# Kernel optimization log

Hardware: AMD Instinct MI355X
Metric: run time of the kernel (lower is better)

## Reference

```python
import jax, jax.numpy as jnp
import numpy as np

B, L, N, P = 64, 512, 321, 720   # batch, seq_len, enc_in, pred_len
E, R, CID, H = 8, 32, 32, 64     # experts, rank, channel_identity_dim, router hidden


def setup_inputs() -> dict:
    key = jax.random.key(0)
    ks = jax.random.split(key, 9)
    return {
        "x": jax.random.normal(ks[0], (B, L, N), dtype=jnp.float32),
        # per-channel identity embedding for the router
        "ident": jax.random.normal(ks[1], (N, CID), dtype=jnp.float32) * 0.02,
        # router MLP: CID -> H -> E
        "rw1": jax.random.normal(ks[2], (CID, H), dtype=jnp.float32) * (1.0 / np.sqrt(CID)),
        "rb1": jnp.zeros((H,), dtype=jnp.float32),
        "rw2": jax.random.normal(ks[3], (H, E), dtype=jnp.float32) * (1.0 / np.sqrt(H)),
        "rb2": jnp.zeros((E,), dtype=jnp.float32),
        # low-rank experts: L -> R -> P
        "w1": jax.random.normal(ks[4], (E, L, R), dtype=jnp.float32) * (1.0 / np.sqrt(L)),
        "w2": jax.random.normal(ks[5], (E, R, P), dtype=jnp.float32) * (1.0 / np.sqrt(R)),
        "b": jnp.zeros((E, P), dtype=jnp.float32),
    }


def reference(x, ident, rw1, rb1, rw2, rb2, w1, w2, b):
    # RevIN-style normalization over the time dim (torch std is unbiased, ddof=1)
    mean = jnp.mean(x, axis=1, keepdims=True)                    # [B,1,N]
    std = jnp.std(x, axis=1, keepdims=True, ddof=1) + 1e-6       # [B,1,N]
    xn = ((x - mean) / std).transpose(0, 2, 1)                   # [B,N,L]

    # per-channel MoE router (soft routing over experts)
    hidden = jax.nn.relu(ident @ rw1 + rb1)                      # [N,H]
    gate = jax.nn.softmax(hidden @ rw2 + rb2, axis=-1)           # [N,E]

    # low-rank expert projections L -> R -> P
    h = jnp.einsum('bnl,elr->bner', xn, w1)                      # [B,N,E,R]
    y = jnp.einsum('bner,erp->bnep', h, w2) + b                  # [B,N,E,P]
    y = jnp.einsum('bnep,ne->bnp', y, gate)                      # [B,N,P]

    pred = y.transpose(0, 2, 1)                                  # [B,P,N]
    return pred * std + mean
```

## Files before the change

kernel.cpp:

```cpp
#include <hip/hip_runtime.h>
#include <math.h>

#define B_ 64
#define L_ 512
#define N_ 321
#define P_ 720
#define E_ 8
#define R_ 32
#define CID_ 32
#define H_ 64
#define ER_ 256
#define KB2 288

typedef __attribute__((ext_vector_type(8))) short bf16x8;
typedef __attribute__((ext_vector_type(4))) float f32x4;
typedef __attribute__((ext_vector_type(8))) unsigned short u16x8;
typedef __attribute__((ext_vector_type(4))) unsigned short u16x4;

#define OFF_GATE 0
#define OFF_CS1  (N_*E_)
#define OFF_W1K  (OFF_CS1 + ER_)
#define OFF_W2X  (OFF_W1K + ER_*L_/2)

__device__ __forceinline__ unsigned short f2bf(float f) {
    unsigned u = __float_as_uint(f);
    u += 0x7fffu + ((u >> 16) & 1u);
    return (unsigned short)(u >> 16);
}
__device__ __forceinline__ float bf2f(unsigned short h) {
    return __uint_as_float(((unsigned)h) << 16);
}

__global__ void router_kernel(const float* __restrict__ ident,
                              const float* __restrict__ rw1, const float* __restrict__ rb1,
                              const float* __restrict__ rw2, const float* __restrict__ rb2,
                              float* __restrict__ gate) {
    int n = blockIdx.x;
    int t = threadIdx.x;
    __shared__ float hid[H_];
    __shared__ float lg[E_];
    float acc = rb1[t];
    #pragma unroll
    for (int c = 0; c < CID_; ++c)
        acc = fmaf(ident[n*CID_ + c], rw1[c*H_ + t], acc);
    hid[t] = fmaxf(acc, 0.f);
    __syncthreads();
    if (t < E_) {
        float a = rb2[t];
        #pragma unroll
        for (int h = 0; h < H_; ++h) a = fmaf(hid[h], rw2[h*E_ + t], a);
        lg[t] = a;
    }
    __syncthreads();
    if (t == 0) {
        float m = lg[0];
        #pragma unroll
        for (int e = 1; e < E_; ++e) m = fmaxf(m, lg[e]);
        float s = 0.f, ex[E_];
        #pragma unroll
        for (int e = 0; e < E_; ++e) { ex[e] = expf(lg[e] - m); s += ex[e]; }
        float inv = 1.f / s;
        #pragma unroll
        for (int e = 0; e < E_; ++e) gate[n*E_ + e] = ex[e] * inv;
    }
}

__global__ void prep_kernel(const float* __restrict__ w1, const float* __restrict__ w2,
                            const float* __restrict__ bias,
                            unsigned short* __restrict__ w1k, unsigned short* __restrict__ w2x,
                            float* __restrict__ cs1) {
    __shared__ float red[16][32];
    int bid = blockIdx.x, t = threadIdx.x;
    if (bid < 256) {
        int g = bid*512 + t;
        int er = g >> 9, l = g & 511;
        w1k[g] = f2bf(w1[(size_t)(er >> 5)*(L_*R_) + (size_t)l*R_ + (er & 31)]);
    } else if (bid < 256 + 720) {
        int p = bid - 256;
        if (t < KB2) {
            unsigned short v;
            if (t < ER_)            v = f2bf(w2[(size_t)t*P_ + p]);
            else if (t < ER_ + E_)  v = f2bf(bias[(size_t)(t - ER_)*P_ + p]);
            else if (t == ER_ + E_) v = 0x3f80;
            else                    v = 0;
            w2x[(size_t)p*KB2 + t] = v;
        }
    } else {
        int e = bid - 976;
        int q = t >> 5, r = t & 31;
        float s = 0.f;
        for (int l = q; l < L_; l += 16)
            s += bf2f(f2bf(w1[(size_t)e*(L_*R_) + (size_t)l*R_ + r]));
        red[q][r] = s;
        __syncthreads();
        if (q == 0) {
            #pragma unroll
            for (int qq = 1; qq < 16; ++qq) s += red[qq][r];
            cs1[e*32 + r] = s;
        }
    }
}

#define HG_STRIDE 296
#define SM_AS   0
#define SM_BS   40960
#define SM_RED  51200
#define SM_MSD  55296
#define SM_OUT  40960
#define SM_TOT  75776

__global__ __launch_bounds__(512, 4) void fused_kernel(
        const float* __restrict__ x, const unsigned short* __restrict__ w1k,
        const unsigned short* __restrict__ w2x, const float* __restrict__ gate,
        const float* __restrict__ cs1, float* __restrict__ out) {
    __shared__ __align__(16) char smem[SM_TOT];
    unsigned short* As  = (unsigned short*)(smem + SM_AS);
    unsigned short* Bs  = (unsigned short*)(smem + SM_BS);
    float* red1 = (float*)(smem + SM_RED);
    float* red2 = red1 + 512;
    float* meanS = (float*)(smem + SM_MSD);
    float* sdS   = meanS + 64;
    unsigned short* hgt = (unsigned short*)(smem + SM_AS);

    const int n0 = blockIdx.x * 64;
    const int b  = blockIdx.y;
    const int tid = threadIdx.x;
    const int lane = tid & 63;
    const int wave = tid >> 6;
    const int wm = wave >> 1;
    const int wn = wave & 1;
    const int l15 = lane & 15;
    const int kgrp = lane >> 4;

    const int arow = tid >> 1;
    const int acol = (tid & 1) * 16;
    const int xn  = tid & 63;
    const int xkb = wave * 4;
    const float* xb = x + (size_t)b * L_ * N_;
    const int gn = n0 + xn;
    const bool nvalid = (gn < N_);

    float s1 = 0.f, s2 = 0.f;
    float xr[3][4];
    u16x8 ar[2][2];

    f32x4 acc[4][2];
    #pragma unroll
    for (int i = 0; i < 4; ++i)
        #pragma unroll
        for (int j = 0; j < 2; ++j) acc[i][j] = (f32x4){0.f,0.f,0.f,0.f};

#define LOADX(s_, t_) { const int k0 = (t_)*32;                                  \
    _Pragma("unroll")                                                            \
    for (int i_ = 0; i_ < 4; ++i_)                                               \
        xr[s_][i_] = nvalid ? xb[(size_t)(k0 + xkb + i_)*N_ + gn] : 0.f; }
#define LOADA(s_, t_) { const int k0 = (t_)*32;                                  \
    ar[s_][0] = *(const u16x8*)&w1k[(size_t)arow*L_ + k0 + acol];                \
    ar[s_][1] = *(const u16x8*)&w1k[(size_t)arow*L_ + k0 + acol + 8]; }
#define STAGE(nb_, xs_, as_) {                                                   \
    *(u16x8*)&As[(size_t)((nb_)*256 + arow)*40 + acol]     = ar[as_][0];         \
    *(u16x8*)&As[(size_t)((nb_)*256 + arow)*40 + acol + 8] = ar[as_][1];         \
    u16x4 bp_;                                                                   \
    _Pragma("unroll")                                                            \
    for (int i_ = 0; i_ < 4; ++i_) {                                             \
        float v_ = xr[xs_][i_]; s1 += v_; s2 = fmaf(v_, v_, s2);                 \
        bp_[i_] = f2bf(v_); }                                                    \
    *(u16x4*)&Bs[(size_t)((nb_)*64 + xn)*40 + xkb] = bp_; }

    LOADX(0, 0); LOADA(0, 0);
    LOADX(1, 1); LOADA(1, 1);
    LOADX(2, 2);
    STAGE(0, 0, 0);
    __syncthreads();

    #pragma unroll
    for (int t = 0; t < 16; ++t) {
        if (t + 3 < 16) LOADX((t + 3) % 3, t + 3);
        if (t + 2 < 16) LOADA((t + 2) & 1, t + 2);
        const int cur = t & 1;
        bf16x8 af[4], bfv[2];
        #pragma unroll
        for (int fm = 0; fm < 4; ++fm)
            af[fm] = *(const bf16x8*)&As[(size_t)(cur*256 + wm*64 + fm*16 + l15)*40 + kgrp*8];
        #pragma unroll
        for (int fn = 0; fn < 2; ++fn)
            bfv[fn] = *(const bf16x8*)&Bs[(size_t)(cur*64 + wn*32 + fn*16 + l15)*40 + kgrp*8];
        #pragma unroll
        for (int fm = 0; fm < 4; ++fm)
            #pragma unroll
            for (int fn = 0; fn < 2; ++fn)
                acc[fm][fn] = __builtin_amdgcn_mfma_f32_16x16x32_bf16(af[fm], bfv[fn], acc[fm][fn], 0, 0, 0);
        if (t < 15) STAGE((t + 1) & 1, (t + 1) % 3, (t + 1) & 1);
        __syncthreads();
    }

    red1[wave*64 + xn] = s1;
    red2[wave*64 + xn] = s2;
    __syncthreads();
    if (tid < 64) {
        float a = 0.f, q = 0.f;
        #pragma unroll
        for (int kk = 0; kk < 8; ++kk) { a += red1[kk*64 + tid]; q += red2[kk*64 + tid]; }
        float mean = a * (1.f/L_);
        float var = (q - (float)L_*mean*mean) * (1.f/(L_-1));
        var = fmaxf(var, 0.f);
        meanS[tid] = mean;
        sdS[tid]   = sqrtf(var) + 1e-6f;
    }
    __syncthreads();

    #pragma unroll
    for (int fm = 0; fm < 4; ++fm) {
        int er0 = wm*64 + fm*16 + kgrp*4;
        int e = er0 >> 5;
        f32x4 c4 = *(const f32x4*)&cs1[er0];
        #pragma unroll
        for (int fn = 0; fn < 2; ++fn) {
            int nl = wn*32 + fn*16 + l15;
            int gnn = n0 + nl; if (gnn > N_-1) gnn = N_-1;
            float g = gate[gnn*E_ + e];
            float m = meanS[nl];
            u16x4 pk;
            #pragma unroll
            for (int j = 0; j < 4; ++j)
                pk[j] = f2bf(g * (acc[fm][fn][j] - m * c4[j]));
            *(u16x4*)&hgt[(size_t)nl*HG_STRIDE + er0] = pk;
        }
    }
    {
        int nl = tid >> 3, seg = tid & 7;
        int gnn = n0 + nl; if (gnn > N_-1) gnn = N_-1;
        float sd = sdS[nl], m = meanS[nl];
        u16x4 pk;
        #pragma unroll
        for (int jj = 0; jj < 4; ++jj) {
            int k = seg*4 + jj;
            float v = (k < E_) ? gate[gnn*E_ + k] * sd : ((k == E_) ? m : 0.f);
            pk[jj] = f2bf(v);
        }
        *(u16x4*)&hgt[(size_t)nl*HG_STRIDE + ER_ + seg*4] = pk;
    }
    __syncthreads();

    float* patch = (float*)(smem + SM_OUT) + wave * 1088;
    for (int pt = wave; pt < 23; pt += 8) {
        const int p0w = pt * 32;
        int pr0 = p0w + l15;       if (pr0 > P_-1) pr0 = P_-1;
        int pr1 = p0w + 16 + l15;  if (pr1 > P_-1) pr1 = P_-1;
        const unsigned short* ap0 = w2x + (size_t)pr0*KB2;
        const unsigned short* ap1 = w2x + (size_t)pr1*KB2;

        f32x4 o[2][4];
        #pragma unroll
        for (int i = 0; i < 2; ++i)
            #pragma unroll
            for (int j = 0; j < 4; ++j) o[i][j] = (f32x4){0.f,0.f,0.f,0.f};

        #pragma unroll
        for (int ks = 0; ks < 9; ++ks) {
            bf16x8 a0f = *(const bf16x8*)&ap0[ks*32 + kgrp*8];
            bf16x8 a1f = *(const bf16x8*)&ap1[ks*32 + kgrp*8];
            bf16x8 bfr[4];
            #pragma unroll
            for (int fn = 0; fn < 4; ++fn)
                bfr[fn] = *(const bf16x8*)&hgt[(size_t)(fn*16 + l15)*HG_STRIDE + ks*32 + kgrp*8];
            #pragma unroll
            for (int fn = 0; fn < 4; ++fn) {
                o[0][fn] = __builtin_amdgcn_mfma_f32_16x16x32_bf16(a0f, bfr[fn], o[0][fn], 0, 0, 0);
                o[1][fn] = __builtin_amdgcn_mfma_f32_16x16x32_bf16(a1f, bfr[fn], o[1][fn], 0, 0, 0);
            }
        }

        #pragma unroll
        for (int fp = 0; fp < 2; ++fp) {
            #pragma unroll
            for (int fn = 0; fn < 4; ++fn)
                #pragma unroll
                for (int j = 0; j < 4; ++j)
                    patch[(kgrp*4 + j)*68 + fn*16 + l15] = o[fp][fn][j];
            __builtin_amdgcn_s_waitcnt(0);
            #pragma unroll
            for (int s = 0; s < 4; ++s) {
                int prow = p0w + fp*16 + 4*s + kgrp;
                f32x4 v = *(const f32x4*)&patch[(4*s + kgrp)*68 + l15*4];
                int nn = n0 + l15*4;
                if (prow < P_) {
                    float* orow = out + ((size_t)b*P_ + prow)*N_;
                    if (nn + 3 < N_) {
                        *(f32x4*)&orow[nn] = v;
                    } else {
                        #pragma unroll
                        for (int q = 0; q < 4; ++q)
                            if (nn + q < N_) orow[nn + q] = v[q];
                    }
                }
            }
        }
    }
#undef LOADX
#undef LOADA
#undef STAGE
}

extern "C" void kernel_launch(void* const* d_in, const int* in_sizes, int n_in,
                              void* d_out, int out_size, void* d_ws, size_t ws_size,
                              hipStream_t stream) {
    const float* x     = (const float*)d_in[0];
    const float* ident = (const float*)d_in[1];
    const float* rw1   = (const float*)d_in[2];
    const float* rb1   = (const float*)d_in[3];
    const float* rw2   = (const float*)d_in[4];
    const float* rb2   = (const float*)d_in[5];
    const float* w1    = (const float*)d_in[6];
    const float* w2    = (const float*)d_in[7];
    const float* bias  = (const float*)d_in[8];
    float* out = (float*)d_out;
    float* ws  = (float*)d_ws;

    float* gate = ws + OFF_GATE;
    float* cs1  = ws + OFF_CS1;
    unsigned short* w1k = (unsigned short*)(ws + OFF_W1K);
    unsigned short* w2x = (unsigned short*)(ws + OFF_W2X);

    router_kernel<<<N_, 64, 0, stream>>>(ident, rw1, rb1, rw2, rb2, gate);
    prep_kernel<<<256 + 720 + 8, 512, 0, stream>>>(w1, w2, bias, w1k, w2x, cs1);
    fused_kernel<<<dim3((N_+63)/64, B_), 512, 0, stream>>>(x, w1k, w2x, gate, cs1, out);
}
```

Before: 69.83 us.

## Swap MFMA operands to store output directly, shrink LDS, remap blocks per XCD

Swaps the A/B operands of the second-stage MFMA so each lane's accumulator holds four consecutive channels. The results can then be written to global memory as float4 without an LDS transpose patch. This removes the patch buffer and overlaps the reduction scratch with the B staging area, cutting LDS from about 74KB to 50KB, and raises launch bounds to 6 blocks per CU. It also flattens the grid and maps blocks so that each XCD handles a contiguous set of batches, which should improve L2 locality. The register pressure of the higher occupancy target may cause spills.

```diff
diff --git a/kernel.cpp b/kernel.cpp
--- a/kernel.cpp
+++ b/kernel.cpp
@@ -104,26 +104,27 @@
 #define HG_STRIDE 296
 #define SM_AS   0
 #define SM_BS   40960
-#define SM_RED  51200
-#define SM_MSD  55296
-#define SM_OUT  40960
-#define SM_TOT  75776
-
-__global__ __launch_bounds__(512, 4) void fused_kernel(
+#define SM_TOT  51200
+
+__global__ __launch_bounds__(512, 6) void fused_kernel(
         const float* __restrict__ x, const unsigned short* __restrict__ w1k,
         const unsigned short* __restrict__ w2x, const float* __restrict__ gate,
         const float* __restrict__ cs1, float* __restrict__ out) {
     __shared__ __align__(16) char smem[SM_TOT];
     unsigned short* As  = (unsigned short*)(smem + SM_AS);
     unsigned short* Bs  = (unsigned short*)(smem + SM_BS);
-    float* red1 = (float*)(smem + SM_RED);
-    float* red2 = red1 + 512;
-    float* meanS = (float*)(smem + SM_MSD);
+    float* red1  = (float*)(smem + SM_BS);
+    float* red2  = red1 + 512;
+    float* meanS = (float*)(smem + SM_BS + 4096);
     float* sdS   = meanS + 64;
     unsigned short* hgt = (unsigned short*)(smem + SM_AS);
 
-    const int n0 = blockIdx.x * 64;
-    const int b  = blockIdx.y;
+    const int bid = blockIdx.x;
+    const int xcd = bid & 7;
+    const int idx = bid >> 3;
+    const int b   = (xcd << 3) + idx / 6;
+    const int n0  = (idx % 6) * 64;
+
     const int tid = threadIdx.x;
     const int lane = tid & 63;
     const int wave = tid >> 6;
@@ -242,13 +243,12 @@
     }
     __syncthreads();
 
-    float* patch = (float*)(smem + SM_OUT) + wave * 1088;
     for (int pt = wave; pt < 23; pt += 8) {
         const int p0w = pt * 32;
         int pr0 = p0w + l15;       if (pr0 > P_-1) pr0 = P_-1;
         int pr1 = p0w + 16 + l15;  if (pr1 > P_-1) pr1 = P_-1;
-        const unsigned short* ap0 = w2x + (size_t)pr0*KB2;
-        const unsigned short* ap1 = w2x + (size_t)pr1*KB2;
+        const unsigned short* bp0 = w2x + (size_t)pr0*KB2;
+        const unsigned short* bp1 = w2x + (size_t)pr1*KB2;
 
         f32x4 o[2][4];
         #pragma unroll
@@ -258,40 +258,33 @@
 
         #pragma unroll
         for (int ks = 0; ks < 9; ++ks) {
-            bf16x8 a0f = *(const bf16x8*)&ap0[ks*32 + kgrp*8];
-            bf16x8 a1f = *(const bf16x8*)&ap1[ks*32 + kgrp*8];
-            bf16x8 bfr[4];
+            bf16x8 b0f = *(const bf16x8*)&bp0[ks*32 + kgrp*8];
+            bf16x8 b1f = *(const bf16x8*)&bp1[ks*32 + kgrp*8];
+            bf16x8 afr[4];
             #pragma unroll
             for (int fn = 0; fn < 4; ++fn)
-                bfr[fn] = *(const bf16x8*)&hgt[(size_t)(fn*16 + l15)*HG_STRIDE + ks*32 + kgrp*8];
+                afr[fn] = *(const bf16x8*)&hgt[(size_t)(fn*16 + l15)*HG_STRIDE + ks*32 + kgrp*8];
             #pragma unroll
             for (int fn = 0; fn < 4; ++fn) {
-                o[0][fn] = __builtin_amdgcn_mfma_f32_16x16x32_bf16(a0f, bfr[fn], o[0][fn], 0, 0, 0);
-                o[1][fn] = __builtin_amdgcn_mfma_f32_16x16x32_bf16(a1f, bfr[fn], o[1][fn], 0, 0, 0);
+                o[0][fn] = __builtin_amdgcn_mfma_f32_16x16x32_bf16(afr[fn], b0f, o[0][fn], 0, 0, 0);
+                o[1][fn] = __builtin_amdgcn_mfma_f32_16x16x32_bf16(afr[fn], b1f, o[1][fn], 0, 0, 0);
             }
         }
 
         #pragma unroll
         for (int fp = 0; fp < 2; ++fp) {
-            #pragma unroll
-            for (int fn = 0; fn < 4; ++fn)
+            int p = p0w + fp*16 + l15;
+            if (p < P_) {
+                float* orow = out + ((size_t)b*P_ + p)*N_;
                 #pragma unroll
-                for (int j = 0; j < 4; ++j)
-                    patch[(kgrp*4 + j)*68 + fn*16 + l15] = o[fp][fn][j];
-            __builtin_amdgcn_s_waitcnt(0);
-            #pragma unroll
-            for (int s = 0; s < 4; ++s) {
-                int prow = p0w + fp*16 + 4*s + kgrp;
-                f32x4 v = *(const f32x4*)&patch[(4*s + kgrp)*68 + l15*4];
-                int nn = n0 + l15*4;
-                if (prow < P_) {
-                    float* orow = out + ((size_t)b*P_ + prow)*N_;
-                    if (nn + 3 < N_) {
-                        *(f32x4*)&orow[nn] = v;
+                for (int fn = 0; fn < 4; ++fn) {
+                    int n = n0 + fn*16 + kgrp*4;
+                    if (n + 3 < N_) {
+                        *(f32x4*)&orow[n] = o[fp][fn];
                     } else {
                         #pragma unroll
-                        for (int q = 0; q < 4; ++q)
-                            if (nn + q < N_) orow[nn + q] = v[q];
+                        for (int j = 0; j < 4; ++j)
+                            if (n + j < N_) orow[n + j] = o[fp][fn][j];
                     }
                 }
             }
@@ -324,5 +317,5 @@
 
     router_kernel<<<N_, 64, 0, stream>>>(ident, rw1, rb1, rw2, rb2, gate);
     prep_kernel<<<256 + 720 + 8, 512, 0, stream>>>(w1, w2, bias, w1k, w2x, cs1);
-    fused_kernel<<<dim3((N_+63)/64, B_), 512, 0, stream>>>(x, w1k, w2x, gate, cs1, out);
-}
+    fused_kernel<<<dim3(6*B_), 512, 0, stream>>>(x, w1k, w2x, gate, cs1, out);
+}
```

Result: slower. 244.1 us (+249.5%).
